# Performance work log

Hardware: AMD Instinct MI355X
Metric: run time of the kernel (lower is better)

Reference implementation:

```python
import jax, jax.numpy as jnp
import numpy as np

B, T, N, D = 4, 24, 325, 512


def setup_inputs() -> dict:
    key = jax.random.key(0)
    ks = jax.random.split(key, 8)
    s = 1.0 / np.sqrt(D)
    return {
        "X": jax.random.normal(ks[0], (B, T, N, D), jnp.float32),
        "Q": jax.random.normal(ks[1], (B, T, N, D), jnp.float32),
        "K": jax.random.normal(ks[2], (B, T, N, D), jnp.float32),
        "V": jax.random.normal(ks[3], (B, T, N, D), jnp.float32),
        "W_head": jax.random.normal(ks[4], (3, D, D), jnp.float32) * s,
        "bias": jax.random.normal(ks[5], (3, D), jnp.float32) * 0.02,
        "W_out": jax.random.normal(ks[6], (D, D), jnp.float32) * s,
        "ln_gamma": jnp.ones((D,), jnp.float32),
        "ln_beta": jnp.zeros((D,), jnp.float32),
        "n_head": 8,
    }


def reference(X, Q, K, V, W_head, bias, W_out, ln_gamma, ln_beta, n_head):
    b, t, n, d = X.shape
    d_k = d // n_head  # num_per_head

    def proj(inp, W, bvec):
        y = jnp.einsum('btnd,de->btne', inp, W) + bvec
        # torch: view(b,T,N,d_k,n_head).permute(-1,0,1,2,3) -> (h,b,t,n,d_k)
        y = y.reshape(b, t, n, d_k, n_head)
        return jnp.transpose(y, (4, 0, 1, 2, 3))

    q = proj(Q, W_head[0], bias[0])
    k = proj(K, W_head[1], bias[1])
    v = proj(V, W_head[2], bias[2])

    scores = jnp.einsum('hbtnd,hbtmd->hbtnm', q, k) / jnp.sqrt(jnp.asarray(d_k, X.dtype))
    attn = jax.nn.softmax(scores, axis=-1)
    o = jnp.einsum('hbtnm,hbtmd->hbtnd', attn, v)
    # inverse of the head split: (h,b,t,n,d_k) -> (b,t,n,d_k,h) -> (b,t,n,d)
    o = jnp.transpose(o, (1, 2, 3, 4, 0)).reshape(b, t, n, d)

    out = jnp.einsum('btnd,de->btne', o, W_out) + X  # out-proj + residual
    mu = jnp.mean(out, axis=-1, keepdims=True)
    var = jnp.mean(jnp.square(out - mu), axis=-1, keepdims=True)
    out = (out - mu) * jax.lax.rsqrt(var + 1e-5) * ln_gamma + ln_beta
    return out
```

## Files before the change

### kernel.cpp

```cpp
#include <hip/hip_runtime.h>
#include <hip/hip_bf16.h>
#include <stdint.h>

#define BB 4
#define TT 24
#define NN 325
#define DD 512
#define NH 8
#define DKH 64
#define MROWS (BB*TT*NN)
#define BTC (BB*TT)

typedef __attribute__((ext_vector_type(4))) float f32x4;
typedef __attribute__((ext_vector_type(8))) short s16x8;
typedef __attribute__((ext_vector_type(4))) unsigned int u32x4;
typedef __attribute__((ext_vector_type(2))) unsigned int u32x2;

__device__ __forceinline__ unsigned short f2bf(float f) {
    union { float f; unsigned int u; } x; x.f = f;
    unsigned int u = x.u;
    u += 0x7fffu + ((u >> 16) & 1u);
    return (unsigned short)(u >> 16);
}
__device__ __forceinline__ unsigned int cvt2(float a, float b) {
    unsigned int r;
    asm("v_cvt_pk_bf16_f32 %0, %1, %2" : "=v"(r) : "v"(a), "v"(b));
    return r;
}
__device__ __forceinline__ unsigned short bf1(float a) {
    return (unsigned short)cvt2(a, a);
}
__device__ __forceinline__ float bf2f(unsigned int u16) {
    union { float f; unsigned int u; } x; x.u = u16 << 16; return x.f;
}

__device__ __forceinline__ void gload16(const void* g, void* l) {
    __builtin_amdgcn_global_load_lds((const __attribute__((address_space(1))) void*)g,
                                     (__attribute__((address_space(3))) void*)l, 16, 0, 0);
}

#define MEMFENCE asm volatile("" ::: "memory")

__global__ void prep_kernel(const float* __restrict__ Wh, const float* __restrict__ bias,
                            const float* __restrict__ Wo,
                            unsigned short* __restrict__ WtH, unsigned short* __restrict__ WtO,
                            float* __restrict__ biasp)
{
    int idx = blockIdx.x * 256 + threadIdx.x;
    if (idx < 3*512*512) {
        int i = idx >> 18; int rem = idx & 262143;
        int cp = rem >> 9; int e = rem & 511;
        int c = ((cp & 63) << 3) | (cp >> 6);
        WtH[idx] = f2bf(Wh[(i << 18) + (e << 9) + c]);
        return;
    }
    int idx2 = idx - 3*512*512;
    if (idx2 >= 0 && idx2 < 512*512) {
        int c = idx2 >> 9; int ep = idx2 & 511;
        int row = ((ep & 63) << 3) | (ep >> 6);
        WtO[idx2] = f2bf(Wo[(row << 9) + c]);
        return;
    }
    int idx3 = idx2 - 512*512;
    if (idx3 >= 0 && idx3 < 3*512) {
        int i = idx3 >> 9; int cp = idx3 & 511;
        int c = ((cp & 63) << 3) | (cp >> 6);
        biasp[idx3] = bias[(i << 9) + c];
    }
}

__global__ __launch_bounds__(256) void projf_gemm3(
    const float* __restrict__ A0, const float* __restrict__ A1, const float* __restrict__ A2,
    const unsigned short* __restrict__ Wt, const float* __restrict__ biasp,
    unsigned short* __restrict__ Y0, unsigned short* __restrict__ Y1, unsigned short* __restrict__ Y2)
{
    __shared__ __align__(16) unsigned short Sh[4*128*64];

    int orig = blockIdx.x;
    int wg = (orig & 7) * 366 + (orig >> 3);
    int z = wg / 976; int rem = wg - z * 976;
    int mtile = rem >> 2; int ntile = rem & 3;

    const float* Ap = (z == 0) ? A0 : ((z == 1) ? A1 : A2);
    unsigned short* Y = (z == 0) ? Y0 : ((z == 1) ? Y1 : Y2);
    const unsigned short* Btn = Wt + z * 512 * 512 + ntile * 128 * 512;
    const float* bias = biasp + z * 512;

    int t = threadIdx.x;
    int wid = t >> 6, lane = t & 63;
    int wm = wid >> 1, wn = wid & 1;
    int lm = lane & 15, lg = lane >> 4;

    long mbase = (long)mtile * 128;

    int tr = t >> 4, tc = t & 15;
    long aoffg[8];
    int awr[8];
    #pragma unroll
    for (int i = 0; i < 8; ++i) {
        int rl = i * 16 + tr;
        long rg = mbase + rl; if (rg >= MROWS) rg = MROWS - 1;
        aoffg[i] = rg * 512 + tc * 4;
        awr[i] = rl * 16 + (((tc >> 1) ^ (rl & 7)) << 1) + (tc & 1);
    }
    int boff[4];
    #pragma unroll
    for (int r = 0; r < 4; ++r) {
        int G = ((r * 4 + wid) << 6) + lane;
        int row = G >> 3;
        int slot = (G & 7) ^ (row & 7);
        boff[r] = row * 512 + slot * 8;
    }

    f32x4 acc[4][4] = {};
    f32x4 ar[3][8];

#define LOADA(kk, S) { const int k0 = (kk) * 64;                               \
    _Pragma("unroll") for (int i = 0; i < 8; ++i)                              \
        ar[S][i] = *(const f32x4*)(Ap + aoffg[i] + k0); }
#define STAGEB(kk, b) { unsigned short* Bs_ = Sh + (b) * 16384 + 8192;         \
    const int k0 = (kk) * 64;                                                  \
    _Pragma("unroll") for (int r = 0; r < 4; ++r)                              \
        gload16(Btn + boff[r] + k0, &Bs_[(r * 4 + wid) << 9]); }
#define DSWA(S, b) { u32x2* dst_ = (u32x2*)(Sh + (b) * 16384);                 \
    _Pragma("unroll") for (int i = 0; i < 8; ++i) {                            \
        u32x2 w_; w_[0] = cvt2(ar[S][i][0], ar[S][i][1]);                      \
        w_[1] = cvt2(ar[S][i][2], ar[S][i][3]); dst_[awr[i]] = w_; } }

    LOADA(0, 0); MEMFENCE;
    STAGEB(0, 0); MEMFENCE;
    asm volatile("s_waitcnt vmcnt(4)" ::: "memory");
    DSWA(0, 0);
    LOADA(1, 1); MEMFENCE;
    STAGEB(1, 1); MEMFENCE;
    LOADA(2, 2); MEMFENCE;

    #pragma unroll
    for (int kk = 0; kk < 8; ++kk) {
        const int b = kk & 1;
        if (kk <= 1)      asm volatile("s_waitcnt vmcnt(20)" ::: "memory");
        else if (kk <= 5) asm volatile("s_waitcnt vmcnt(12)" ::: "memory");
        else if (kk == 6) asm volatile("s_waitcnt vmcnt(4)"  ::: "memory");
        else              asm volatile("s_waitcnt vmcnt(0)"  ::: "memory");
        asm volatile("s_waitcnt lgkmcnt(0)" ::: "memory");
        __builtin_amdgcn_s_barrier();

        if (kk <= 4) { LOADA(kk + 3, (kk + 3) % 3); MEMFENCE; }

        const unsigned short* As = Sh + b * 16384;
        const unsigned short* Bs = As + 8192;
        #pragma unroll
        for (int ks = 0; ks < 2; ++ks) {
            s16x8 afr[4], bfr[4];
            #pragma unroll
            for (int mf = 0; mf < 4; ++mf) {
                int row = wm * 64 + mf * 16 + lm;
                afr[mf] = ((const s16x8*)As)[row * 8 + ((ks * 4 + lg) ^ (row & 7))];
            }
            #pragma unroll
            for (int nf = 0; nf < 4; ++nf) {
                int row = wn * 64 + nf * 16 + lm;
                bfr[nf] = ((const s16x8*)Bs)[row * 8 + ((ks * 4 + lg) ^ (row & 7))];
            }
            #pragma unroll
            for (int mf = 0; mf < 4; ++mf)
                #pragma unroll
                for (int nf = 0; nf < 4; ++nf)
                    acc[mf][nf] = __builtin_amdgcn_mfma_f32_16x16x32_bf16(afr[mf], bfr[nf], acc[mf][nf], 0, 0, 0);
        }
        MEMFENCE;
        __builtin_amdgcn_s_barrier();
        if (kk <= 5) { STAGEB(kk + 2, b); MEMFENCE; }
        if (kk <= 6) { DSWA((kk + 1) % 3, b ^ 1); }
    }
#undef LOADA
#undef STAGEB
#undef DSWA

    __syncthreads();
    #pragma unroll
    for (int nf = 0; nf < 4; ++nf) {
        int col = wn * 64 + nf * 16 + lm;
        float bv = bias[ntile * 128 + col];
        #pragma unroll
        for (int mf = 0; mf < 4; ++mf) {
            #pragma unroll
            for (int j = 0; j < 4; ++j) {
                int row = wm * 64 + mf * 16 + lg * 4 + j;
                Sh[row * 128 + (col ^ ((row & 12) << 2))] = bf1(acc[mf][nf][j] + bv);
            }
        }
    }
    __syncthreads();
    #pragma unroll
    for (int it = 0; it < 8; ++it) {
        int row = it * 16 + (t >> 4);
        int c8 = (t & 15) * 8;
        u32x4 v = *(const u32x4*)&Sh[row * 128 + (c8 ^ ((row & 12) << 2))];
        long grow = mbase + row;
        if (grow < MROWS)
            *(u32x4*)&Y[grow * 512 + ntile * 128 + c8] = v;
    }
}

__global__ __launch_bounds__(256) void out_gemm(
    const unsigned short* __restrict__ A, const unsigned short* __restrict__ Bt,
    const float* __restrict__ X, unsigned short* __restrict__ Out)
{
    __shared__ __align__(16) unsigned short Sh[4*128*64];

    int orig = blockIdx.x;
    int wg = (orig & 7) * 122 + (orig >> 3);
    int mtile = wg >> 2; int ntile = wg & 3;

    int t = threadIdx.x;
    int wid = t >> 6, lane = t & 63;
    int wm = wid >> 1, wn = wid & 1;
    int lm = lane & 15, lg = lane >> 4;

    long mbase = (long)mtile * 128;
    const unsigned short* Abase = A + mbase * 512;
    const unsigned short* Btn = Bt + ntile * 128 * 512;

    int aoff[4], boff[4];
    #pragma unroll
    for (int r = 0; r < 4; ++r) {
        int G = ((r * 4 + wid) << 6) + lane;
        int row = G >> 3;
        int slot = (G & 7) ^ (row & 7);
        int rowc = row;
        if (mbase + row > MROWS - 1) rowc = (int)(MROWS - 1 - mbase);
        aoff[r] = rowc * 512 + slot * 8;
        boff[r] = row * 512 + slot * 8;
    }

    f32x4 acc[4][4] = {};

    auto STAGE = [&](int kk, int b) {
        unsigned short* As = Sh + b * 16384;
        unsigned short* Bs = As + 8192;
        const int k0 = kk * 64;
        #pragma unroll
        for (int r = 0; r < 4; ++r)
            gload16(Abase + aoff[r] + k0, &As[(r * 4 + wid) << 9]);
        #pragma unroll
        for (int r = 0; r < 4; ++r)
            gload16(Btn + boff[r] + k0, &Bs[(r * 4 + wid) << 9]);
    };

    STAGE(0, 0);
    STAGE(1, 1);

    #pragma unroll
    for (int kk = 0; kk < 8; ++kk) {
        const int b = kk & 1;
        if (kk < 7) asm volatile("s_waitcnt vmcnt(8)" ::: "memory");
        else        asm volatile("s_waitcnt vmcnt(0)" ::: "memory");
        __builtin_amdgcn_s_barrier();

        const unsigned short* As = Sh + b * 16384;
        const unsigned short* Bs = As + 8192;
        #pragma unroll
        for (int ks = 0; ks < 2; ++ks) {
            s16x8 afr[4], bfr[4];
            #pragma unroll
            for (int mf = 0; mf < 4; ++mf) {
                int row = wm * 64 + mf * 16 + lm;
                afr[mf] = ((const s16x8*)As)[row * 8 + ((ks * 4 + lg) ^ (row & 7))];
            }
            #pragma unroll
            for (int nf = 0; nf < 4; ++nf) {
                int row = wn * 64 + nf * 16 + lm;
                bfr[nf] = ((const s16x8*)Bs)[row * 8 + ((ks * 4 + lg) ^ (row & 7))];
            }
            #pragma unroll
            for (int mf = 0; mf < 4; ++mf)
                #pragma unroll
                for (int nf = 0; nf < 4; ++nf)
                    acc[mf][nf] = __builtin_amdgcn_mfma_f32_16x16x32_bf16(afr[mf], bfr[nf], acc[mf][nf], 0, 0, 0);
        }
        MEMFENCE;
        __builtin_amdgcn_s_barrier();
        if (kk + 2 < 8) STAGE(kk + 2, b);
    }

    __syncthreads();
    #pragma unroll
    for (int nf = 0; nf < 4; ++nf) {
        int col = wn * 64 + nf * 16 + lm;
        #pragma unroll
        for (int mf = 0; mf < 4; ++mf) {
            #pragma unroll
            for (int j = 0; j < 4; ++j) {
                int row = wm * 64 + mf * 16 + lg * 4 + j;
                Sh[row * 128 + (col ^ ((row & 12) << 2))] = bf1(acc[mf][nf][j]);
            }
        }
    }
    __syncthreads();
    #pragma unroll
    for (int it = 0; it < 8; ++it) {
        int row = it * 16 + (t >> 4);
        int c8 = (t & 15) * 8;
        u32x4 v = *(const u32x4*)&Sh[row * 128 + (c8 ^ ((row & 12) << 2))];
        long grow = mbase + row;
        if (grow < MROWS) {
            long gidx = grow * 512 + ntile * 128 + c8;
            const float* xp = X + gidx;
            f32x4 x0 = *(const f32x4*)xp, x1 = *(const f32x4*)(xp + 4);
            float xx[8] = {x0[0], x0[1], x0[2], x0[3], x1[0], x1[1], x1[2], x1[3]};
            u32x4 o;
            #pragma unroll
            for (int q = 0; q < 4; ++q) {
                float lo = bf2f(v[q] & 0xffffu) + xx[2 * q];
                float hi = bf2f(v[q] >> 16)     + xx[2 * q + 1];
                o[q] = cvt2(lo, hi);
            }
            *(u32x4*)&Out[gidx] = o;
        }
    }
}

#define SCALE2 0.18033688f

__global__ __launch_bounds__(256) void attn_kernel(
    const unsigned short* __restrict__ Qw, const unsigned short* __restrict__ Kw,
    const unsigned short* __restrict__ Vw, unsigned short* __restrict__ Ow)
{
    __shared__ __align__(16) unsigned short Qs[128*64];
    __shared__ __align__(16) unsigned short Ks[64*64];
    __shared__ __align__(16) unsigned short Vts[64*64];
    __shared__ __align__(16) unsigned short Ps[4][16*64];

    int bid = blockIdx.x;
    int x = bid & 7, s = bid >> 3;
    int qc = s % 3;
    int gi = s / 3;
    int g  = x + 8 * gi;
    int h  = g & 7, bt = g >> 3;

    int t = threadIdx.x;
    int wid = t >> 6, lane = t & 63, lm = lane & 15, lg = lane >> 4;

    long rowbase = (long)bt * NN;
    int colbase = h * 64;
    int q0 = qc * 128;

    {
        int i = t >> 1, half = t & 1;
        int rowc = q0 + i; if (rowc > NN - 1) rowc = NN - 1;
        const u32x4* src = (const u32x4*)(Qw + (rowbase + rowc) * 512 + colbase);
        u32x4* dst = (u32x4*)Qs;
        #pragma unroll
        for (int ss = 0; ss < 4; ++ss) {
            int slot = half * 4 + ss;
            dst[i * 8 + (slot ^ (i & 7))] = src[slot];
        }
    }
    __syncthreads();
    s16x8 aq[2][2];
    #pragma unroll
    for (int qs = 0; qs < 2; ++qs) {
        int row = qs * 64 + wid * 16 + lm;
        aq[qs][0] = ((const s16x8*)Qs)[row * 8 + ((0 + lg) ^ (row & 7))];
        aq[qs][1] = ((const s16x8*)Qs)[row * 8 + ((4 + lg) ^ (row & 7))];
    }

    f32x4 oacc[2][4] = {};
    float lsum[2][4] = {};

    for (int tile = 0; tile < 6; ++tile) {
        const int kv0 = tile * 64;
        __syncthreads();
        #pragma unroll
        for (int r = 0; r < 2; ++r) {
            int G = r * 256 + t;
            int row = G >> 3;
            int slot = (G & 7) ^ (row & 7);
            int rowg = kv0 + row; if (rowg > NN - 1) rowg = NN - 1;
            gload16(Kw + (rowbase + rowg) * 512 + colbase + slot * 8, &Ks[G * 8]);
        }
        {
            int i = t >> 2, quarter = t & 3;
            int rowc = kv0 + i; if (rowc > NN - 1) rowc = NN - 1;
            const u32x4* src = (const u32x4*)(Vw + (rowbase + rowc) * 512 + colbase + quarter * 16);
            unsigned short vb[16] __attribute__((aligned(16)));
            *((u32x4*)vb) = src[0];
            *((u32x4*)(vb + 8)) = src[1];
            #pragma unroll
            for (int e = 0; e < 16; ++e) {
                int dk = quarter * 16 + e;
                int sv = (dk & 7) ^ ((dk >> 3) & 7);
                Vts[dk * 64 + (i ^ (sv << 3))] = vb[e];
            }
        }
        asm volatile("s_waitcnt vmcnt(0)" ::: "memory");
        __syncthreads();

        const bool tail = (tile == 5);
        #pragma unroll
        for (int qs = 0; qs < 2; ++qs) {
            f32x4 sacc[4] = {};
            #pragma unroll
            for (int ks = 0; ks < 2; ++ks) {
                #pragma unroll
                for (int nf = 0; nf < 4; ++nf) {
                    int row = nf * 16 + lm;
                    s16x8 bk = ((const s16x8*)Ks)[row * 8 + ((ks*4 + lg) ^ (row & 7))];
                    sacc[nf] = __builtin_amdgcn_mfma_f32_16x16x32_bf16(aq[qs][ks], bk, sacc[nf], 0, 0, 0);
                }
            }
            #pragma unroll
            for (int nf = 0; nf < 4; ++nf) {
                bool valid = !tail || (kv0 + nf * 16 + lm < NN);
                #pragma unroll
                for (int j = 0; j < 4; ++j) {
                    float pv = valid ? exp2f(sacc[nf][j] * SCALE2) : 0.f;
                    lsum[qs][j] += pv;
                    int r = lg * 4 + j;
                    int col = nf * 16 + lm;
                    Ps[wid][r * 64 + (col ^ (((r >> 1) & 7) << 3))] = bf1(pv);
                }
            }
            #pragma unroll
            for (int ks = 0; ks < 2; ++ks) {
                s16x8 ap = ((const s16x8*)Ps[wid])[lm * 8 + ((ks*4 + lg) ^ ((lm >> 1) & 7))];
                #pragma unroll
                for (int df = 0; df < 4; ++df) {
                    int vrow = df * 16 + lm;
                    int sv = (vrow & 7) ^ ((vrow >> 3) & 7);
                    s16x8 bv = ((const s16x8*)Vts)[vrow * 8 + ((ks*4 + lg) ^ sv)];
                    oacc[qs][df] = __builtin_amdgcn_mfma_f32_16x16x32_bf16(ap, bv, oacc[qs][df], 0, 0, 0);
                }
            }
        }
    }

    #pragma unroll
    for (int qs = 0; qs < 2; ++qs) {
        float inv[4];
        #pragma unroll
        for (int j = 0; j < 4; ++j) {
            float v = lsum[qs][j];
            v += __shfl_xor(v, 1, 16);
            v += __shfl_xor(v, 2, 16);
            v += __shfl_xor(v, 4, 16);
            v += __shfl_xor(v, 8, 16);
            inv[j] = __builtin_amdgcn_rcpf(v);
        }
        #pragma unroll
        for (int df = 0; df < 4; ++df) {
            int dk = df * 16 + lm;
            #pragma unroll
            for (int j = 0; j < 4; ++j) {
                int rloc = q0 + qs * 64 + wid * 16 + lg * 4 + j;
                if (rloc < NN)
                    Ow[(rowbase + rloc) * 512 + colbase + dk] = bf1(oacc[qs][df][j] * inv[j]);
            }
        }
    }
}

__global__ __launch_bounds__(256) void ln_kernel(
    const unsigned short* __restrict__ T, const float* __restrict__ gamma,
    const float* __restrict__ beta, float* __restrict__ Outp)
{
    int wid = threadIdx.x >> 6, lane = threadIdx.x & 63;
    long row = (long)blockIdx.x * 4 + wid;
    s16x8 h = ((const s16x8*)(T + row * 512))[lane];
    float v[8];
    #pragma unroll
    for (int j = 0; j < 8; ++j) v[j] = bf2f((unsigned int)(unsigned short)h[j]);
    float s = 0.f, sq = 0.f;
    #pragma unroll
    for (int j = 0; j < 8; ++j) { s += v[j]; sq += v[j] * v[j]; }
    #pragma unroll
    for (int m = 1; m < 64; m <<= 1) {
        s  += __shfl_xor(s, m);
        sq += __shfl_xor(sq, m);
    }
    float mean = s * (1.f / 512.f);
    float var = sq * (1.f / 512.f) - mean * mean;
    float rstd = rsqrtf(var + 1e-5f);
    const float4* g = (const float4*)gamma;
    const float4* b = (const float4*)beta;
    float4 g0 = g[lane * 2], g1 = g[lane * 2 + 1];
    float4 b0 = b[lane * 2], b1 = b[lane * 2 + 1];
    float4 o0, o1;
    o0.x = (v[0] - mean) * rstd * g0.x + b0.x;
    o0.y = (v[1] - mean) * rstd * g0.y + b0.y;
    o0.z = (v[2] - mean) * rstd * g0.z + b0.z;
    o0.w = (v[3] - mean) * rstd * g0.w + b0.w;
    o1.x = (v[4] - mean) * rstd * g1.x + b1.x;
    o1.y = (v[5] - mean) * rstd * g1.y + b1.y;
    o1.z = (v[6] - mean) * rstd * g1.z + b1.z;
    o1.w = (v[7] - mean) * rstd * g1.w + b1.w;
    float4* dst = (float4*)(Outp + row * 512);
    dst[lane * 2]     = o0;
    dst[lane * 2 + 1] = o1;
}

extern "C" void kernel_launch(void* const* d_in, const int* in_sizes, int n_in,
                              void* d_out, int out_size, void* d_ws, size_t ws_size,
                              hipStream_t stream)
{
    const float* X  = (const float*)d_in[0];
    const float* Q  = (const float*)d_in[1];
    const float* K  = (const float*)d_in[2];
    const float* V  = (const float*)d_in[3];
    const float* Wh = (const float*)d_in[4];
    const float* bi = (const float*)d_in[5];
    const float* Wo = (const float*)d_in[6];
    const float* gamma = (const float*)d_in[7];
    const float* beta  = (const float*)d_in[8];

    char* ws = (char*)d_ws;
    const size_t msz = (size_t)MROWS * 512 * 2;
    unsigned short* q_ws = (unsigned short*)(ws);
    unsigned short* k_ws = (unsigned short*)(ws + msz);
    unsigned short* v_ws = (unsigned short*)(ws + 2 * msz);
    unsigned short* o_ws = (unsigned short*)(ws + 3 * msz);
    unsigned short* WtH  = (unsigned short*)(ws + 4 * msz);
    unsigned short* WtO  = WtH + 3 * 512 * 512;
    float* biasp         = (float*)(ws + 4 * msz + (size_t)4*512*512*2);
    unsigned short* tmpb = q_ws;

    prep_kernel<<<4102, 256, 0, stream>>>(Wh, bi, Wo, WtH, WtO, biasp);

    projf_gemm3<<<2928, 256, 0, stream>>>(Q, K, V, WtH, biasp, q_ws, k_ws, v_ws);

    attn_kernel<<<2304, 256, 0, stream>>>(q_ws, k_ws, v_ws, o_ws);

    out_gemm<<<976, 256, 0, stream>>>(o_ws, WtO, X, tmpb);

    ln_kernel<<<7800, 256, 0, stream>>>(tmpb, gamma, beta, (float*)d_out);
}
```

Measured before the change: 285.5 us.

## Load A fragments directly into registers and shrink projection tile to 64 rows

The QKV projection GEMM now uses a 64x128 tile instead of 128x128. Each wave reads its own 16 rows of fp32 activations straight into registers and converts them to bf16 MFMA operands, so the A operand no longer goes through LDS. Only B is double-buffered in shared memory, which halves LDS use, removes the A store and barrier traffic, and doubles the grid for more occupancy. In exchange, B tiles are reloaded twice as often across blocks, each B fragment feeds only one A fragment, and the global A loads are less coalesced.

```diff
diff --git a/kernel.cpp b/kernel.cpp
--- a/kernel.cpp
+++ b/kernel.cpp
@@ -74,11 +74,11 @@
     const unsigned short* __restrict__ Wt, const float* __restrict__ biasp,
     unsigned short* __restrict__ Y0, unsigned short* __restrict__ Y1, unsigned short* __restrict__ Y2)
 {
-    __shared__ __align__(16) unsigned short Sh[4*128*64];
+    __shared__ __align__(16) unsigned short Bs2[2][128*64];
 
     int orig = blockIdx.x;
-    int wg = (orig & 7) * 366 + (orig >> 3);
-    int z = wg / 976; int rem = wg - z * 976;
+    int wg = (orig & 7) * 732 + (orig >> 3);
+    int z = wg / 1952; int rem = wg - z * 1952;
     int mtile = rem >> 2; int ntile = rem & 3;
 
     const float* Ap = (z == 0) ? A0 : ((z == 1) ? A1 : A2);
@@ -88,112 +88,87 @@
 
     int t = threadIdx.x;
     int wid = t >> 6, lane = t & 63;
-    int wm = wid >> 1, wn = wid & 1;
     int lm = lane & 15, lg = lane >> 4;
 
-    long mbase = (long)mtile * 128;
-
-    int tr = t >> 4, tc = t & 15;
-    long aoffg[8];
-    int awr[8];
-    #pragma unroll
-    for (int i = 0; i < 8; ++i) {
-        int rl = i * 16 + tr;
-        long rg = mbase + rl; if (rg >= MROWS) rg = MROWS - 1;
-        aoffg[i] = rg * 512 + tc * 4;
-        awr[i] = rl * 16 + (((tc >> 1) ^ (rl & 7)) << 1) + (tc & 1);
-    }
+    long mbase = (long)mtile * 64;
+
+    long arow = mbase + wid * 16 + lm;
+    if (arow >= MROWS) arow = MROWS - 1;
+    const float* aptr = Ap + arow * 512 + lg * 8;
+
     int boff[4];
     #pragma unroll
     for (int r = 0; r < 4; ++r) {
-        int G = ((r * 4 + wid) << 6) + lane;
+        int G = r * 256 + t;
         int row = G >> 3;
         int slot = (G & 7) ^ (row & 7);
         boff[r] = row * 512 + slot * 8;
     }
 
-    f32x4 acc[4][4] = {};
-    f32x4 ar[3][8];
+    f32x4 acc[8] = {};
+    f32x4 ar[2][4];
 
 #define LOADA(kk, S) { const int k0 = (kk) * 64;                               \
-    _Pragma("unroll") for (int i = 0; i < 8; ++i)                              \
-        ar[S][i] = *(const f32x4*)(Ap + aoffg[i] + k0); }
-#define STAGEB(kk, b) { unsigned short* Bs_ = Sh + (b) * 16384 + 8192;         \
+    ar[S][0] = *(const f32x4*)(aptr + k0);                                     \
+    ar[S][1] = *(const f32x4*)(aptr + k0 + 4);                                 \
+    ar[S][2] = *(const f32x4*)(aptr + k0 + 32);                                \
+    ar[S][3] = *(const f32x4*)(aptr + k0 + 36); }
+#define STAGEB(kk, b) { unsigned short* Bs_ = Bs2[b];                          \
     const int k0 = (kk) * 64;                                                  \
     _Pragma("unroll") for (int r = 0; r < 4; ++r)                              \
-        gload16(Btn + boff[r] + k0, &Bs_[(r * 4 + wid) << 9]); }
-#define DSWA(S, b) { u32x2* dst_ = (u32x2*)(Sh + (b) * 16384);                 \
-    _Pragma("unroll") for (int i = 0; i < 8; ++i) {                            \
-        u32x2 w_; w_[0] = cvt2(ar[S][i][0], ar[S][i][1]);                      \
-        w_[1] = cvt2(ar[S][i][2], ar[S][i][3]); dst_[awr[i]] = w_; } }
+        gload16(Btn + boff[r] + k0, &Bs_[(r * 256 + t) * 8]); }
 
     LOADA(0, 0); MEMFENCE;
     STAGEB(0, 0); MEMFENCE;
-    asm volatile("s_waitcnt vmcnt(4)" ::: "memory");
-    DSWA(0, 0);
-    LOADA(1, 1); MEMFENCE;
     STAGEB(1, 1); MEMFENCE;
-    LOADA(2, 2); MEMFENCE;
 
     #pragma unroll
     for (int kk = 0; kk < 8; ++kk) {
         const int b = kk & 1;
-        if (kk <= 1)      asm volatile("s_waitcnt vmcnt(20)" ::: "memory");
-        else if (kk <= 5) asm volatile("s_waitcnt vmcnt(12)" ::: "memory");
-        else if (kk == 6) asm volatile("s_waitcnt vmcnt(4)"  ::: "memory");
-        else              asm volatile("s_waitcnt vmcnt(0)"  ::: "memory");
-        asm volatile("s_waitcnt lgkmcnt(0)" ::: "memory");
+        const int s = kk & 1;
+        if (kk == 0 || kk == 7) asm volatile("s_waitcnt vmcnt(4)" ::: "memory");
+        else                    asm volatile("s_waitcnt vmcnt(8)" ::: "memory");
         __builtin_amdgcn_s_barrier();
 
-        if (kk <= 4) { LOADA(kk + 3, (kk + 3) % 3); MEMFENCE; }
-
-        const unsigned short* As = Sh + b * 16384;
-        const unsigned short* Bs = As + 8192;
+        if (kk <= 6) { LOADA(kk + 1, s ^ 1); MEMFENCE; }
+
+        const unsigned short* Bs = Bs2[b];
         #pragma unroll
         for (int ks = 0; ks < 2; ++ks) {
-            s16x8 afr[4], bfr[4];
-            #pragma unroll
-            for (int mf = 0; mf < 4; ++mf) {
-                int row = wm * 64 + mf * 16 + lm;
-                afr[mf] = ((const s16x8*)As)[row * 8 + ((ks * 4 + lg) ^ (row & 7))];
-            }
-            #pragma unroll
-            for (int nf = 0; nf < 4; ++nf) {
-                int row = wn * 64 + nf * 16 + lm;
-                bfr[nf] = ((const s16x8*)Bs)[row * 8 + ((ks * 4 + lg) ^ (row & 7))];
-            }
-            #pragma unroll
-            for (int mf = 0; mf < 4; ++mf)
-                #pragma unroll
-                for (int nf = 0; nf < 4; ++nf)
-                    acc[mf][nf] = __builtin_amdgcn_mfma_f32_16x16x32_bf16(afr[mf], bfr[nf], acc[mf][nf], 0, 0, 0);
+            union { s16x8 h; u32x4 u; } af;
+            af.u[0] = cvt2(ar[s][ks*2][0], ar[s][ks*2][1]);
+            af.u[1] = cvt2(ar[s][ks*2][2], ar[s][ks*2][3]);
+            af.u[2] = cvt2(ar[s][ks*2+1][0], ar[s][ks*2+1][1]);
+            af.u[3] = cvt2(ar[s][ks*2+1][2], ar[s][ks*2+1][3]);
+            #pragma unroll
+            for (int nf = 0; nf < 8; ++nf) {
+                int row = nf * 16 + lm;
+                s16x8 bfr = ((const s16x8*)Bs)[row * 8 + ((ks * 4 + lg) ^ (row & 7))];
+                acc[nf] = __builtin_amdgcn_mfma_f32_16x16x32_bf16(af.h, bfr, acc[nf], 0, 0, 0);
+            }
         }
         MEMFENCE;
         __builtin_amdgcn_s_barrier();
         if (kk <= 5) { STAGEB(kk + 2, b); MEMFENCE; }
-        if (kk <= 6) { DSWA((kk + 1) % 3, b ^ 1); }
     }
 #undef LOADA
 #undef STAGEB
-#undef DSWA
 
     __syncthreads();
-    #pragma unroll
-    for (int nf = 0; nf < 4; ++nf) {
-        int col = wn * 64 + nf * 16 + lm;
+    unsigned short* Sh = Bs2[0];
+    #pragma unroll
+    for (int nf = 0; nf < 8; ++nf) {
+        int col = nf * 16 + lm;
         float bv = bias[ntile * 128 + col];
         #pragma unroll
-        for (int mf = 0; mf < 4; ++mf) {
-            #pragma unroll
-            for (int j = 0; j < 4; ++j) {
-                int row = wm * 64 + mf * 16 + lg * 4 + j;
-                Sh[row * 128 + (col ^ ((row & 12) << 2))] = bf1(acc[mf][nf][j] + bv);
-            }
+        for (int j = 0; j < 4; ++j) {
+            int row = wid * 16 + lg * 4 + j;
+            Sh[row * 128 + (col ^ ((row & 12) << 2))] = bf1(acc[nf][j] + bv);
         }
     }
     __syncthreads();
     #pragma unroll
-    for (int it = 0; it < 8; ++it) {
+    for (int it = 0; it < 4; ++it) {
         int row = it * 16 + (t >> 4);
         int c8 = (t & 15) * 8;
         u32x4 v = *(const u32x4*)&Sh[row * 128 + (c8 ^ ((row & 12) << 2))];
@@ -527,7 +502,7 @@
 
     prep_kernel<<<4102, 256, 0, stream>>>(Wh, bi, Wo, WtH, WtO, biasp);
 
-    projf_gemm3<<<2928, 256, 0, stream>>>(Q, K, V, WtH, biasp, q_ws, k_ws, v_ws);
+    projf_gemm3<<<5856, 256, 0, stream>>>(Q, K, V, WtH, biasp, q_ws, k_ws, v_ws);
 
     attn_kernel<<<2304, 256, 0, stream>>>(q_ws, k_ws, v_ws, o_ws);
 
```

New measurement: 264.7 us. 7.3% less time.
